# Kernel tuning notes

Measured on AMD Instinct MI355X. Metric: run time of the kernel, lower is better.

## Reference

```python
import jax, jax.numpy as jnp
import numpy as np

DIM_MODEL = 1024
NUM_HEADS = 16
HEAD_DIM = DIM_MODEL // NUM_HEADS
NEG = -1000000000.0


def setup_inputs() -> dict:
    key = jax.random.key(0)
    ks = jax.random.split(key, 11)
    B, S, D = 2, 2048, DIM_MODEL
    s = 1.0 / np.sqrt(D)
    return {
        "q": jax.random.normal(ks[0], (B, S, D), jnp.float32),
        "k": jax.random.normal(ks[1], (B, S, D), jnp.float32),
        "v": jax.random.normal(ks[2], (B, S, D), jnp.float32),
        "Wq": jax.random.normal(ks[3], (D, D), jnp.float32) * s,
        "bq": jnp.zeros((D,), jnp.float32),
        "Wk": jax.random.normal(ks[4], (D, D), jnp.float32) * s,
        "bk": jnp.zeros((D,), jnp.float32),
        "Wv": jax.random.normal(ks[5], (D, D), jnp.float32) * s,
        "bv": jnp.zeros((D,), jnp.float32),
        "Wo": jax.random.normal(ks[6], (D, D), jnp.float32) * s,
        "bo": jnp.zeros((D,), jnp.float32),
    }


def reference(q, k, v, Wq, bq, Wk, bk, Wv, bv, Wo, bo):
    B, S, D = q.shape
    H, hd = NUM_HEADS, HEAD_DIM

    def proj(x, W, b):
        # torch Linear: x @ W.T + b, then split heads -> [B, H, S, hd]
        y = jnp.einsum("bsd,ed->bse", x, W) + b
        return y.reshape(B, S, H, hd).transpose(0, 2, 1, 3)

    qh = proj(q, Wq, bq)
    kh = proj(k, Wk, bk)
    vh = proj(v, Wv, bv)

    scores = jnp.einsum("bhqd,bhkd->bhqk", qh, kh) / np.sqrt(hd)
    # torch.triu(ones(S,S), diagonal=0): upper triangle INCLUDING diagonal is masked
    mask = jnp.triu(jnp.ones((S, S), bool))
    scores = jnp.where(mask, NEG, scores)
    # softmax over dim=-2 (query axis), as in the original module
    attn = jax.nn.softmax(scores, axis=-2)
    ctx = jnp.einsum("bhqk,bhkd->bhqd", attn, vh)  # [B,H,S,hd]
    ctx = ctx.transpose(0, 2, 1, 3).reshape(B, S, D)
    return jnp.einsum("bsd,ed->bse", ctx, Wo) + bo
```

## Files before the change

kernel.cpp:

```cpp
#include <hip/hip_runtime.h>

typedef __bf16 bf16;
typedef __attribute__((ext_vector_type(8))) __bf16 bf16x8;
typedef __attribute__((ext_vector_type(2))) __bf16 bf16x2;
typedef __attribute__((ext_vector_type(4))) float f32x4;

#define AS1 __attribute__((address_space(1)))
#define AS3 __attribute__((address_space(3)))

#define BB 2
#define SS 2048
#define DD 1024
#define HH 16
#define HD 64
#define BH (BB*HH)

#define QSCALE 0.1803368801111244f

static __device__ __forceinline__ f32x4 mfma16(bf16x8 a, bf16x8 b, f32x4 c) {
  return __builtin_amdgcn_mfma_f32_16x16x32_bf16(a, b, c, 0, 0, 0);
}
static __device__ __forceinline__ float fexp2(float x) {
  return __builtin_amdgcn_exp2f(x);
}

static __device__ __forceinline__ void swz512(int bid, int& bh, int& pr) {
  int c = bid & 7, j = bid >> 3;
  bh = c + 8 * (j & 3);
  pr = j >> 2;
}
static __device__ __forceinline__ void swz1024(int bid, int& bh, int& strip0, int& qh) {
  int c = bid & 7, j = bid >> 3;
  bh = c + 8 * (j & 3);
  int rem = j >> 2;
  strip0 = rem & 15;
  qh = rem >> 4;
}

__global__ __launch_bounds__(256) void cvt_w(const float* __restrict__ s0, const float* __restrict__ s1,
                                             const float* __restrict__ s2, const float* __restrict__ s3,
                                             bf16* __restrict__ o0, bf16* __restrict__ o1,
                                             bf16* __restrict__ o2, bf16* __restrict__ o3) {
  const int z = blockIdx.y;
  const float* s = (z == 0) ? s0 : (z == 1) ? s1 : (z == 2) ? s2 : s3;
  bf16* o = (z == 0) ? o0 : (z == 1) ? o1 : (z == 2) ? o2 : o3;
  int i = blockIdx.x * 256 + threadIdx.x;
  const float4* sp = (const float4*)s;
  float4 a = sp[2 * i], b = sp[2 * i + 1];
  bf16x8 v;
  v[0] = (bf16)a.x; v[1] = (bf16)a.y; v[2] = (bf16)a.z; v[3] = (bf16)a.w;
  v[4] = (bf16)b.x; v[5] = (bf16)b.y; v[6] = (bf16)b.z; v[7] = (bf16)b.w;
  ((bf16x8*)o)[i] = v;
}

__global__ __launch_bounds__(256) void cvt_x(const float* __restrict__ s0, const float* __restrict__ s1,
                                             const float* __restrict__ s2,
                                             bf16* __restrict__ o0, bf16* __restrict__ o1,
                                             bf16* __restrict__ o2) {
  const int z = blockIdx.y;
  const float* s = (z == 0) ? s0 : (z == 1) ? s1 : s2;
  bf16* o = (z == 0) ? o0 : (z == 1) ? o1 : o2;
  int i = blockIdx.x * 256 + threadIdx.x;
  const float4* sp = (const float4*)s;
  float4 a = sp[2 * i], b = sp[2 * i + 1];
  bf16x8 v;
  v[0] = (bf16)a.x; v[1] = (bf16)a.y; v[2] = (bf16)a.z; v[3] = (bf16)a.w;
  v[4] = (bf16)b.x; v[5] = (bf16)b.y; v[6] = (bf16)b.z; v[7] = (bf16)b.w;
  ((bf16x8*)o)[i] = v;
}

__device__ __forceinline__ void gemm_core(const bf16* __restrict__ A,
                                          const bf16* __restrict__ Bm, int K,
                                          int m0, int n0, int w, int l,
                                          bf16* sA, bf16* sB, f32x4 (&acc)[4][4]) {
  const int l15 = l & 15, lg = l >> 4;
  const int wr = (w >> 1) * 64, wc = (w & 1) * 64;
  for (int kt = 0; kt < K; kt += 32) {
#pragma unroll
    for (int i = 0; i < 2; ++i) {
      int t = i * 256 + w * 64 + l;
      const bf16* ga = A + (size_t)(m0 + (t >> 2)) * K + kt + (t & 3) * 8;
      const bf16* gb = Bm + (size_t)(n0 + (t >> 2)) * K + kt + (t & 3) * 8;
      __builtin_amdgcn_global_load_lds((const AS1 void*)ga,
                                       (AS3 void*)(sA + (i * 256 + w * 64) * 8), 16, 0, 0);
      __builtin_amdgcn_global_load_lds((const AS1 void*)gb,
                                       (AS3 void*)(sB + (i * 256 + w * 64) * 8), 16, 0, 0);
    }
    __syncthreads();
    bf16x8 af[4], bfr[4];
#pragma unroll
    for (int m = 0; m < 4; ++m)
      af[m] = *(const bf16x8*)(sA + (wr + m * 16 + l15) * 32 + lg * 8);
#pragma unroll
    for (int n = 0; n < 4; ++n)
      bfr[n] = *(const bf16x8*)(sB + (wc + n * 16 + l15) * 32 + lg * 8);
#pragma unroll
    for (int m = 0; m < 4; ++m)
#pragma unroll
      for (int n = 0; n < 4; ++n)
        acc[m][n] = mfma16(af[m], bfr[n], acc[m][n]);
    __syncthreads();
  }
}

__global__ __launch_bounds__(256) void proj_gemm(
    const bf16* __restrict__ Xq, const bf16* __restrict__ Xk, const bf16* __restrict__ Xv,
    const bf16* __restrict__ Wq, const bf16* __restrict__ Wk, const bf16* __restrict__ Wv,
    const float* __restrict__ bq, const float* __restrict__ bk, const float* __restrict__ bv,
    bf16* __restrict__ Oq, bf16* __restrict__ Ok, bf16* __restrict__ Ovt) {
  __shared__ __align__(16) bf16 sA[128 * 32];
  __shared__ __align__(16) bf16 sB[128 * 32];
  const int z = blockIdx.z;
  const bf16* A = (z == 0) ? Xq : ((z == 1) ? Xk : Xv);
  const bf16* W = (z == 0) ? Wq : ((z == 1) ? Wk : Wv);
  const float* bias = (z == 0) ? bq : ((z == 1) ? bk : bv);
  const int tid = threadIdx.x, l = tid & 63, w = tid >> 6;
  const int m0 = blockIdx.y * 128, n0 = blockIdx.x * 128;
  f32x4 acc[4][4] = {};
  gemm_core(A, W, DD, m0, n0, w, l, sA, sB, acc);
  const int l15 = l & 15, lg = l >> 4;
  const int wr = (w >> 1) * 64, wc = (w & 1) * 64;
#pragma unroll
  for (int n = 0; n < 4; ++n) {
    int col = n0 + wc + n * 16 + l15;
    float bb = bias[col];
    int h = col >> 6, d = col & 63;
#pragma unroll
    for (int m = 0; m < 4; ++m) {
#pragma unroll
      for (int r = 0; r < 4; ++r) {
        int row = m0 + wr + m * 16 + lg * 4 + r;
        int b = row >> 11, s = row & (SS - 1);
        float vv = acc[m][n][r] + bb;
        if (z == 0) vv *= QSCALE;
        if (z != 2)
          ((z == 0) ? Oq : Ok)[(((size_t)(b * HH + h)) * SS + s) * HD + d] = (bf16)vv;
        else
          Ovt[(((size_t)(b * HH + h)) * HD + d) * SS + s] = (bf16)vv;
      }
    }
  }
}

__global__ __launch_bounds__(256) void out_gemm(const bf16* __restrict__ A,
                                                const bf16* __restrict__ W,
                                                const float* __restrict__ bias,
                                                float* __restrict__ out) {
  __shared__ __align__(16) bf16 sA[128 * 32];
  __shared__ __align__(16) bf16 sB[128 * 32];
  const int tid = threadIdx.x, l = tid & 63, w = tid >> 6;
  const int m0 = blockIdx.y * 128, n0 = blockIdx.x * 128;
  f32x4 acc[4][4] = {};
  gemm_core(A, W, DD, m0, n0, w, l, sA, sB, acc);
  const int l15 = l & 15, lg = l >> 4;
  const int wr = (w >> 1) * 64, wc = (w & 1) * 64;
#pragma unroll
  for (int n = 0; n < 4; ++n) {
    int col = n0 + wc + n * 16 + l15;
    float bb = bias[col];
#pragma unroll
    for (int m = 0; m < 4; ++m)
#pragma unroll
      for (int r = 0; r < 4; ++r) {
        int row = m0 + wr + m * 16 + lg * 4 + r;
        out[(size_t)row * DD + col] = acc[m][n][r] + bb;
      }
  }
}

__global__ __launch_bounds__(256) void colz(const bf16* __restrict__ Qb,
                                            const bf16* __restrict__ Kb,
                                            float* __restrict__ zPart) {
  __shared__ float zred[4][64];
  int bh, pair, qh;
  swz1024(blockIdx.x, bh, pair, qh);
  const int tid = threadIdx.x, l = tid & 63, w = tid >> 6;
  const int l15 = l & 15, lg = l >> 4;
  const bf16* Q = Qb + (size_t)bh * SS * HD;
  const bf16* Kh = Kb + (size_t)bh * SS * HD;

  for (int half = 0; half < 2; ++half) {
    const int s = half ? (31 - pair) : pair;
    const int c0 = s * 64;
    bf16x8 kf[4][2];
#pragma unroll
    for (int kt = 0; kt < 4; ++kt) {
      kf[kt][0] = *(const bf16x8*)&Kh[(c0 + kt * 16 + l15) * HD + lg * 8];
      kf[kt][1] = *(const bf16x8*)&Kh[(c0 + kt * 16 + l15) * HD + 32 + lg * 8];
    }
    float z[4] = {};
    const int qstart = c0 + qh * 64 + w * 16;
    bf16x8 qa0, qa1, qn0, qn1;
    if (qstart < SS) {
      qa0 = *(const bf16x8*)&Q[(qstart + l15) * HD + lg * 8];
      qa1 = *(const bf16x8*)&Q[(qstart + l15) * HD + 32 + lg * 8];
    }
    for (int qb = qstart; qb < SS; qb += 128) {
      const int qnext = qb + 128;
      if (qnext < SS) {
        qn0 = *(const bf16x8*)&Q[(qnext + l15) * HD + lg * 8];
        qn1 = *(const bf16x8*)&Q[(qnext + l15) * HD + 32 + lg * 8];
      }
      f32x4 d[4] = {};
#pragma unroll
      for (int kt = 0; kt < 4; ++kt) {
        d[kt] = mfma16(qa0, kf[kt][0], d[kt]);
        d[kt] = mfma16(qa1, kf[kt][1], d[kt]);
      }
#pragma unroll
      for (int kt = 0; kt < 4; ++kt) {
        const int kcol = c0 + kt * 16 + l15;
#pragma unroll
        for (int r = 0; r < 4; ++r) {
          int qq = qb + lg * 4 + r;
          z[kt] += (qq > kcol) ? fexp2(d[kt][r]) : 0.f;
        }
      }
      qa0 = qn0; qa1 = qn1;
    }
#pragma unroll
    for (int kt = 0; kt < 4; ++kt) {
      z[kt] += __shfl_xor(z[kt], 16);
      z[kt] += __shfl_xor(z[kt], 32);
    }
    if (l < 16) {
#pragma unroll
      for (int kt = 0; kt < 4; ++kt) zred[w][kt * 16 + l15] = z[kt];
    }
    __syncthreads();
    if (tid < 64) {
      float zs = zred[0][tid] + zred[1][tid] + zred[2][tid] + zred[3][tid];
      zPart[((size_t)qh * BH + bh) * SS + c0 + tid] = zs;
    }
    __syncthreads();
  }
}

__global__ __launch_bounds__(256) void rzfin(const float* __restrict__ zPart,
                                             float* __restrict__ cRZ) {
  int i = blockIdx.x * 256 + threadIdx.x;
  f32x4 a = ((const f32x4*)zPart)[i];
  f32x4 b = ((const f32x4*)(zPart + (size_t)BH * SS))[i];
  f32x4 r;
#pragma unroll
  for (int j = 0; j < 4; ++j) {
    float s = a[j] + b[j];
    r[j] = (s > 0.f) ? 1.0f / s : 0.f;
  }
  ((f32x4*)cRZ)[i] = r;
}

__global__ __launch_bounds__(256) void vscale(bf16* __restrict__ Vt,
                                              const float* __restrict__ cRZ,
                                              float* __restrict__ vlastB) {
  int i = blockIdx.x * 256 + threadIdx.x;
  int sc = i & (SS / 8 - 1);
  int rest = i >> 8;
  int s0 = sc * 8;
  bf16* p = Vt + (size_t)rest * SS + s0;
  const float* rz = cRZ + (size_t)(rest >> 6) * SS + s0;
  bf16x8 v = *(const bf16x8*)p;
  if (s0 + 8 == SS) vlastB[rest] = (float)v[7] * (1.0f / (float)SS);
  f32x4 r0 = *(const f32x4*)rz, r1 = *(const f32x4*)(rz + 4);
  bf16x8 o;
#pragma unroll
  for (int j = 0; j < 4; ++j) o[j] = (bf16)((float)v[j] * r0[j]);
#pragma unroll
  for (int j = 0; j < 4; ++j) o[4 + j] = (bf16)((float)v[4 + j] * r1[j]);
  *(bf16x8*)p = o;
}

struct KV {
  bf16x8 k[4];
  unsigned int v[4][4];
};

static __device__ __forceinline__ void kv_load(KV& b, const bf16* __restrict__ Kh,
                                               const bf16* __restrict__ V, int k0,
                                               int l15, int lg) {
  b.k[0] = *(const bf16x8*)&Kh[(k0 + l15) * HD + lg * 8];
  b.k[1] = *(const bf16x8*)&Kh[(k0 + l15) * HD + 32 + lg * 8];
  b.k[2] = *(const bf16x8*)&Kh[(k0 + 16 + l15) * HD + lg * 8];
  b.k[3] = *(const bf16x8*)&Kh[(k0 + 16 + l15) * HD + 32 + lg * 8];
#pragma unroll
  for (int dt = 0; dt < 4; ++dt) {
    const bf16* vrow = &V[(size_t)(dt * 16 + l15) * SS];
    uint2 lo = *(const uint2*)&vrow[k0 + 4 * lg];
    uint2 hi = *(const uint2*)&vrow[k0 + 16 + 4 * lg];
    b.v[dt][0] = lo.x; b.v[dt][1] = lo.y; b.v[dt][2] = hi.x; b.v[dt][3] = hi.y;
  }
}

template <bool DIAG>
static __device__ __forceinline__ void kv_compute(const KV& b, int k0, int q0,
                                                  const bf16x8 (&qa)[4][2],
                                                  f32x4 (&acc)[4][4], int l15, int lg) {
  const int kb0i = k0 + lg * 4, kb1i = k0 + 16 + lg * 4;
#pragma unroll
  for (int qt = 0; qt < 4; ++qt) {
    f32x4 s0 = {}, s1 = {};
    s0 = mfma16(b.k[0], qa[qt][0], s0);
    s0 = mfma16(b.k[1], qa[qt][1], s0);
    s1 = mfma16(b.k[2], qa[qt][0], s1);
    s1 = mfma16(b.k[3], qa[qt][1], s1);
    const int qq = q0 + qt * 16 + l15;
    union { unsigned int u[4]; bf16x8 v; } pa;
#pragma unroll
    for (int hw = 0; hw < 2; ++hw) {
      bf16x2 t0, t1;
#pragma unroll
      for (int r = 0; r < 2; ++r) {
        int rr = hw * 2 + r;
        float p0 = fexp2(s0[rr]);
        float p1 = fexp2(s1[rr]);
        if (DIAG) {
          p0 = (kb0i + rr < qq) ? p0 : 0.f;
          p1 = (kb1i + rr < qq) ? p1 : 0.f;
        }
        t0[r] = (bf16)p0;
        t1[r] = (bf16)p1;
      }
      pa.u[hw] = __builtin_bit_cast(unsigned int, t0);
      pa.u[hw + 2] = __builtin_bit_cast(unsigned int, t1);
    }
#pragma unroll
    for (int dt = 0; dt < 4; ++dt) {
      union { unsigned int u[4]; bf16x8 v; } vf;
      vf.u[0] = b.v[dt][0]; vf.u[1] = b.v[dt][1];
      vf.u[2] = b.v[dt][2]; vf.u[3] = b.v[dt][3];
      acc[qt][dt] = mfma16(pa.v, vf.v, acc[qt][dt]);
    }
  }
}

__global__ __launch_bounds__(256, 2) void attn_ctx(const bf16* __restrict__ Qb,
                                                   const bf16* __restrict__ Kb,
                                                   const bf16* __restrict__ Vt,
                                                   const float* __restrict__ vlastB,
                                                   bf16* __restrict__ ctx) {
  __shared__ __align__(16) float red[3][64 * 68];
  int bh, pr;
  swz512(blockIdx.x, bh, pr);
  const int tid = threadIdx.x, l = tid & 63, w = tid >> 6;
  const int l15 = l & 15, lg = l >> 4;
  const bf16* Q = Qb + (size_t)bh * SS * HD;
  const bf16* Kh = Kb + (size_t)bh * SS * HD;
  const bf16* V = Vt + (size_t)bh * HD * SS;
  const int b = bh >> 4, h = bh & 15;

  float vlast[4];
#pragma unroll
  for (int dt = 0; dt < 4; ++dt) vlast[dt] = vlastB[bh * 64 + dt * 16 + l15];

  for (int half = 0; half < 2; ++half) {
    const int t = half ? (31 - pr) : pr;
    const int q0 = t * 64;

    bf16x8 qa[4][2];
#pragma unroll
    for (int qt = 0; qt < 4; ++qt)
#pragma unroll
      for (int kk = 0; kk < 2; ++kk)
        qa[qt][kk] = *(const bf16x8*)&Q[(q0 + qt * 16 + l15) * HD + kk * 32 + lg * 8];

    f32x4 acc[4][4] = {};
    KV A, B;
    int k0 = w * 32;
    if (k0 < q0) {
      kv_load(A, Kh, V, k0, l15, lg);
      for (;;) {
        int kn = k0 + 128;
        if (kn >= q0) { kv_compute<false>(A, k0, q0, qa, acc, l15, lg); break; }
        kv_load(B, Kh, V, kn, l15, lg);
        kv_compute<false>(A, k0, q0, qa, acc, l15, lg);
        k0 = kn; kn += 128;
        if (kn >= q0) { kv_compute<false>(B, k0, q0, qa, acc, l15, lg); break; }
        kv_load(A, Kh, V, kn, l15, lg);
        kv_compute<false>(B, k0, q0, qa, acc, l15, lg);
        k0 = kn;
      }
    }
    {
      const int cw = (2 * t) & 3;
      int dk = (w == cw) ? q0 : ((w == ((cw + 1) & 3)) ? q0 + 32 : -1);
      if (dk >= 0) {
        kv_load(A, Kh, V, dk, l15, lg);
        kv_compute<true>(A, dk, q0, qa, acc, l15, lg);
      }
    }

    if (w) {
      float* buf = red[w - 1];
#pragma unroll
      for (int qt = 0; qt < 4; ++qt)
#pragma unroll
        for (int dt = 0; dt < 4; ++dt)
          *(f32x4*)&buf[(dt * 16 + l15) * 68 + qt * 16 + lg * 4] = acc[qt][dt];
    }
    __syncthreads();
    if (w == 0) {
#pragma unroll
      for (int qt = 0; qt < 4; ++qt) {
#pragma unroll
        for (int dt = 0; dt < 4; ++dt) {
          f32x4 a = acc[qt][dt];
#pragma unroll
          for (int j = 0; j < 3; ++j)
            a += *(const f32x4*)&red[j][(dt * 16 + l15) * 68 + qt * 16 + lg * 4];
#pragma unroll
          for (int r = 0; r < 4; ++r) {
            int q = q0 + qt * 16 + lg * 4 + r;
            ctx[((size_t)(b * SS + q)) * DD + h * HD + dt * 16 + l15] =
                (bf16)(a[r] + vlast[dt]);
          }
        }
      }
    }
    __syncthreads();
  }
}

extern "C" void kernel_launch(void* const* d_in, const int* in_sizes, int n_in,
                              void* d_out, int out_size, void* d_ws, size_t ws_size,
                              hipStream_t stream) {
  const float* q  = (const float*)d_in[0];
  const float* k  = (const float*)d_in[1];
  const float* v  = (const float*)d_in[2];
  const float* Wq = (const float*)d_in[3];
  const float* bq = (const float*)d_in[4];
  const float* Wk = (const float*)d_in[5];
  const float* bk = (const float*)d_in[6];
  const float* Wv = (const float*)d_in[7];
  const float* bv = (const float*)d_in[8];
  const float* Wo = (const float*)d_in[9];
  const float* bo = (const float*)d_in[10];

  char* ws = (char*)d_ws;
  const size_t SZP = (size_t)4096 * 1024 * 2;
  const size_t SZW = (size_t)1024 * 1024 * 2;
  bf16* Qb   = (bf16*)(ws + 0 * SZP);
  bf16* Kb   = (bf16*)(ws + 1 * SZP);
  bf16* Vt   = (bf16*)(ws + 2 * SZP);
  bf16* ctxb = (bf16*)(ws + 3 * SZP);
  bf16* qb16 = (bf16*)(ws + 4 * SZP);
  bf16* kb16 = (bf16*)(ws + 5 * SZP);
  bf16* vb16 = (bf16*)(ws + 6 * SZP);
  bf16* Wqb  = (bf16*)(ws + 7 * SZP + 0 * SZW);
  bf16* Wkb  = (bf16*)(ws + 7 * SZP + 1 * SZW);
  bf16* Wvb  = (bf16*)(ws + 7 * SZP + 2 * SZW);
  bf16* Wob  = (bf16*)(ws + 7 * SZP + 3 * SZW);
  float* zPart = (float*)(ws + 7 * SZP + 4 * SZW);
  float* cRZ   = zPart + (size_t)2 * BH * SS;
  float* vlastB = cRZ + (size_t)BH * SS;

  cvt_w<<<dim3(512, 4), 256, 0, stream>>>(Wq, Wk, Wv, Wo, Wqb, Wkb, Wvb, Wob);
  cvt_x<<<dim3(2048, 3), 256, 0, stream>>>(q, k, v, qb16, kb16, vb16);

  proj_gemm<<<dim3(1024 / 128, 4096 / 128, 3), 256, 0, stream>>>(
      qb16, kb16, vb16, Wqb, Wkb, Wvb, bq, bk, bv, Qb, Kb, Vt);

  colz<<<1024, 256, 0, stream>>>(Qb, Kb, zPart);
  rzfin<<<(BH * SS / 4) / 256, 256, 0, stream>>>(zPart, cRZ);
  vscale<<<(BH * HD * SS / 8) / 256, 256, 0, stream>>>(Vt, cRZ, vlastB);
  attn_ctx<<<512, 256, 0, stream>>>(Qb, Kb, Vt, vlastB, ctxb);

  out_gemm<<<dim3(1024 / 128, 4096 / 128), 256, 0, stream>>>(ctxb, Wob, bo, (float*)d_out);
}
```

Baseline: 174.5 us.

## Double attn_ctx waves to eight per block with tree reduction over LDS

The attention-context kernel now launches 512 threads (8 waves) per block instead of 4, so each wave walks the key range with a stride of 256 and the causal diagonal blocks are spread across 8 waves. The manual double-buffered K/V prefetch loop becomes a simple single-buffer load-then-compute loop. Partial accumulators are combined with a three-stage tree reduction through a larger LDS buffer instead of wave 0 summing three buffers. This trades more parallelism per block for extra barriers, more LDS, register pressure under the 512x4 launch bound, and no software prefetch.

```diff
diff --git a/kernel.cpp b/kernel.cpp
--- a/kernel.cpp
+++ b/kernel.cpp
@@ -333,12 +333,12 @@
   }
 }
 
-__global__ __launch_bounds__(256, 2) void attn_ctx(const bf16* __restrict__ Qb,
+__global__ __launch_bounds__(512, 4) void attn_ctx(const bf16* __restrict__ Qb,
                                                    const bf16* __restrict__ Kb,
                                                    const bf16* __restrict__ Vt,
                                                    const float* __restrict__ vlastB,
                                                    bf16* __restrict__ ctx) {
-  __shared__ __align__(16) float red[3][64 * 68];
+  __shared__ __align__(16) float red[4][64 * 68];
   int bh, pr;
   swz512(blockIdx.x, bh, pr);
   const int tid = threadIdx.x, l = tid & 63, w = tid >> 6;
@@ -364,33 +364,22 @@
         qa[qt][kk] = *(const bf16x8*)&Q[(q0 + qt * 16 + l15) * HD + kk * 32 + lg * 8];
 
     f32x4 acc[4][4] = {};
-    KV A, B;
-    int k0 = w * 32;
-    if (k0 < q0) {
+    KV A;
+    for (int k0 = w * 32; k0 < q0; k0 += 256) {
       kv_load(A, Kh, V, k0, l15, lg);
-      for (;;) {
-        int kn = k0 + 128;
-        if (kn >= q0) { kv_compute<false>(A, k0, q0, qa, acc, l15, lg); break; }
-        kv_load(B, Kh, V, kn, l15, lg);
-        kv_compute<false>(A, k0, q0, qa, acc, l15, lg);
-        k0 = kn; kn += 128;
-        if (kn >= q0) { kv_compute<false>(B, k0, q0, qa, acc, l15, lg); break; }
-        kv_load(A, Kh, V, kn, l15, lg);
-        kv_compute<false>(B, k0, q0, qa, acc, l15, lg);
-        k0 = kn;
-      }
+      kv_compute<false>(A, k0, q0, qa, acc, l15, lg);
     }
     {
-      const int cw = (2 * t) & 3;
-      int dk = (w == cw) ? q0 : ((w == ((cw + 1) & 3)) ? q0 + 32 : -1);
+      const int cw = (2 * t) & 7;
+      int dk = (w == cw) ? q0 : ((w == ((cw + 1) & 7)) ? q0 + 32 : -1);
       if (dk >= 0) {
         kv_load(A, Kh, V, dk, l15, lg);
         kv_compute<true>(A, dk, q0, qa, acc, l15, lg);
       }
     }
 
-    if (w) {
-      float* buf = red[w - 1];
+    if (w >= 4) {
+      float* buf = red[w - 4];
 #pragma unroll
       for (int qt = 0; qt < 4; ++qt)
 #pragma unroll
@@ -398,15 +387,46 @@
           *(f32x4*)&buf[(dt * 16 + l15) * 68 + qt * 16 + lg * 4] = acc[qt][dt];
     }
     __syncthreads();
+    if (w < 4) {
+#pragma unroll
+      for (int qt = 0; qt < 4; ++qt)
+#pragma unroll
+        for (int dt = 0; dt < 4; ++dt)
+          acc[qt][dt] += *(const f32x4*)&red[w][(dt * 16 + l15) * 68 + qt * 16 + lg * 4];
+    }
+    __syncthreads();
+    if (w == 2 || w == 3) {
+      float* buf = red[w - 2];
+#pragma unroll
+      for (int qt = 0; qt < 4; ++qt)
+#pragma unroll
+        for (int dt = 0; dt < 4; ++dt)
+          *(f32x4*)&buf[(dt * 16 + l15) * 68 + qt * 16 + lg * 4] = acc[qt][dt];
+    }
+    __syncthreads();
+    if (w < 2) {
+#pragma unroll
+      for (int qt = 0; qt < 4; ++qt)
+#pragma unroll
+        for (int dt = 0; dt < 4; ++dt)
+          acc[qt][dt] += *(const f32x4*)&red[w][(dt * 16 + l15) * 68 + qt * 16 + lg * 4];
+    }
+    __syncthreads();
+    if (w == 1) {
+#pragma unroll
+      for (int qt = 0; qt < 4; ++qt)
+#pragma unroll
+        for (int dt = 0; dt < 4; ++dt)
+          *(f32x4*)&red[0][(dt * 16 + l15) * 68 + qt * 16 + lg * 4] = acc[qt][dt];
+    }
+    __syncthreads();
     if (w == 0) {
 #pragma unroll
       for (int qt = 0; qt < 4; ++qt) {
 #pragma unroll
         for (int dt = 0; dt < 4; ++dt) {
           f32x4 a = acc[qt][dt];
-#pragma unroll
-          for (int j = 0; j < 3; ++j)
-            a += *(const f32x4*)&red[j][(dt * 16 + l15) * 68 + qt * 16 + lg * 4];
+          a += *(const f32x4*)&red[0][(dt * 16 + l15) * 68 + qt * 16 + lg * 4];
 #pragma unroll
           for (int r = 0; r < 4; ++r) {
             int q = q0 + qt * 16 + lg * 4 + r;
@@ -462,7 +482,7 @@
   colz<<<1024, 256, 0, stream>>>(Qb, Kb, zPart);
   rzfin<<<(BH * SS / 4) / 256, 256, 0, stream>>>(zPart, cRZ);
   vscale<<<(BH * HD * SS / 8) / 256, 256, 0, stream>>>(Vt, cRZ, vlastB);
-  attn_ctx<<<512, 256, 0, stream>>>(Qb, Kb, Vt, vlastB, ctxb);
+  attn_ctx<<<512, 512, 0, stream>>>(Qb, Kb, Vt, vlastB, ctxb);
 
   out_gemm<<<dim3(1024 / 128, 4096 / 128), 256, 0, stream>>>(ctxb, Wob, bo, (float*)d_out);
 }
```

After: 205.6 us. 17.8% more time.
